# Kernel tuning notes

Hardware: AMD Instinct MI355X
Metric: run time of the kernel (lower is better)

## Reference

```python
import jax, jax.numpy as jnp
import numpy as np

R = 14        # num_relations
N = 100000    # num nodes
E = 1600000   # num edges
B = 8         # n_bases: num_blocks for layer 1, num_bases for layer 2
DIN, DH, DOUT = 64, 64, 64


def setup_inputs() -> dict:
    key = jax.random.key(0)
    ks = jax.random.split(key, 10)
    x = jax.random.normal(ks[0], (N, DIN), jnp.float32)
    edge_index = jax.random.randint(ks[1], (2, E), 0, N)
    edge_type = jax.random.randint(ks[2], (E,), 0, R)
    # Layer 1: block-diagonal decomposition weights (R, B, DIN/B, DH/B)
    w1 = jax.random.normal(ks[3], (R, B, DIN // B, DH // B), jnp.float32) * 0.1
    root1 = jax.random.normal(ks[4], (DIN, DH), jnp.float32) * 0.1
    bias1 = jnp.zeros((DH,), jnp.float32)
    # Layer 2: basis decomposition: W_r = sum_b comp2[r,b] * bases2[b]
    comp2 = jax.random.normal(ks[5], (R, B), jnp.float32) * 0.3
    bases2 = jax.random.normal(ks[6], (B, DH, DOUT), jnp.float32) * 0.1
    root2 = jax.random.normal(ks[7], (DH, DOUT), jnp.float32) * 0.1
    bias2 = jnp.zeros((DOUT,), jnp.float32)
    return {"x": x, "edge_index": edge_index, "edge_type": edge_type,
            "w1": w1, "root1": root1, "bias1": bias1,
            "comp2": comp2, "bases2": bases2, "root2": root2, "bias2": bias2}


def _rel_scatter_max(h_rel, src, dst, edge_type):
    """h_rel: (R, N, d) per-relation transformed node features.
    Per-relation scatter-max over destination nodes, then sum over relations
    (PyG RGCNConv with aggr='max': empty segments contribute 0)."""
    msgs = h_rel[edge_type, src]                  # (E, d) gather
    seg = edge_type * N + dst                     # combined (relation, dst) key
    agg = jax.ops.segment_max(msgs, seg, num_segments=R * N)  # (R*N, d), -inf where empty
    agg = jnp.where(jnp.isneginf(agg), 0.0, agg)
    return agg.reshape(R, N, -1).sum(axis=0)      # (N, d)


def reference(x, edge_index, edge_type, w1, root1, bias1, comp2, bases2, root2, bias2):
    src, dst = edge_index[0], edge_index[1]
    # ---- layer 1: block-diagonal RGCNConv, aggr='max' ----
    xb = x.reshape(N, B, DIN // B)
    h = jnp.einsum('nbi,rbio->rnbo', xb, w1).reshape(R, N, DH)
    out = _rel_scatter_max(h, src, dst, edge_type) + x @ root1 + bias1
    x1 = jax.nn.relu(out)  # dropout p=0.4 is identity in eval mode
    # ---- layer 2: basis-decomposed RGCNConv, aggr='max' ----
    W2 = jnp.einsum('rb,bio->rio', comp2, bases2)  # (R, DH, DOUT)
    h2 = jnp.einsum('ni,rio->rno', x1, W2)         # (R, N, DOUT)
    out2 = _rel_scatter_max(h2, src, dst, edge_type) + x1 @ root2 + bias2
    return out2
```

## Files before the change

kernel.cpp:

```cpp
#include <hip/hip_runtime.h>
#include <math.h>

#define RNUM 14
#define NNODE 100000
#define ENUM 1600000
#define NBKT 196
#define NFINE 8192
#define NBLK1 ((ENUM + 8191) / 8192)
#define NT16 (NNODE / 16)
#define NTB ((NT16 + 15) / 16)
#define FRAGREL (RNUM + 1)
#define FRAGTOT (2 * FRAGREL * 4096)

typedef __attribute__((ext_vector_type(8))) short bf16x8;
typedef __attribute__((ext_vector_type(4))) float f32x4;

__device__ inline unsigned short f2bf(float f) {
    unsigned u = __builtin_bit_cast(unsigned, f);
    u += 0x7FFF + ((u >> 16) & 1);
    return (unsigned short)(u >> 16);
}
__device__ inline float bf2f(unsigned short h) {
    unsigned u = ((unsigned)h) << 16;
    return __builtin_bit_cast(float, u);
}
__device__ inline int uload(const int* __restrict__ p) {
    return __builtin_amdgcn_readfirstlane(*p);
}

__global__ void __launch_bounds__(1024) bhist_k(const int* __restrict__ dst,
                                                int* __restrict__ bcnt) {
    __shared__ int c[256];
    int t = threadIdx.x;
    if (t < 256) c[t] = 0;
    __syncthreads();
    int e0 = blockIdx.x * 8192;
#pragma unroll
    for (int j = 0; j < 8; j++) {
        int e = e0 + j * 1024 + t;
        if (e < ENUM) atomicAdd(&c[dst[e] >> 9], 1);
    }
    __syncthreads();
    if (t < NBKT && c[t] > 0) atomicAdd(&bcnt[t], c[t]);
}

__global__ void bscan_k(const int* __restrict__ bcnt, int* __restrict__ bbase,
                        int* __restrict__ bcursor) {
    __shared__ int sh[256];
    int t = threadIdx.x;
    int v = (t < NBKT) ? bcnt[t] : 0;
    sh[t] = v;
    __syncthreads();
    for (int o = 1; o < 256; o <<= 1) {
        int u = (t >= o) ? sh[t - o] : 0;
        __syncthreads();
        sh[t] += u;
        __syncthreads();
    }
    int excl = sh[t] - v;
    if (t < NBKT) { bbase[t] = excl; bcursor[t] = excl; }
    if (t == NBKT - 1) bbase[NBKT] = sh[t];
}

__global__ void __launch_bounds__(1024) scatter1_k(const int* __restrict__ src,
        const int* __restrict__ dst, const int* __restrict__ et,
        int* __restrict__ bcursor, int2* __restrict__ pay) {
    __shared__ int cnt[256];
    __shared__ int rnk[256];
    __shared__ int base[256];
    int t = threadIdx.x;
    if (t < 256) { cnt[t] = 0; rnk[t] = 0; }
    __syncthreads();
    int e0 = blockIdx.x * 8192;
    int d[8], s[8], r[8];
#pragma unroll
    for (int j = 0; j < 8; j++) {
        int e = e0 + j * 1024 + t;
        if (e < ENUM) {
            d[j] = dst[e]; s[j] = src[e]; r[j] = et[e];
            atomicAdd(&cnt[d[j] >> 9], 1);
        } else d[j] = -1;
    }
    __syncthreads();
    if (t < NBKT && cnt[t] > 0) base[t] = atomicAdd(&bcursor[t], cnt[t]);
    __syncthreads();
#pragma unroll
    for (int j = 0; j < 8; j++) {
        if (d[j] < 0) continue;
        int b = d[j] >> 9;
        int rk = atomicAdd(&rnk[b], 1);
        int2 p; p.x = r[j] * NNODE + s[j]; p.y = (d[j] & 511) * 16 + r[j];
        pay[base[b] + rk] = p;
    }
}

__global__ void __launch_bounds__(1024) bsort_k(const int2* __restrict__ pay,
        const int* __restrict__ bbase, int* __restrict__ offs, int* __restrict__ ssrc) {
    __shared__ int cnt[NFINE];
    __shared__ int tsum[1024];
    int bkt = blockIdx.x, t = threadIdx.x;
    int e0 = bbase[bkt], e1 = bbase[bkt + 1];
#pragma unroll
    for (int i = t; i < NFINE; i += 1024) cnt[i] = 0;
    __syncthreads();
    for (int e = e0 + t; e < e1; e += 1024) atomicAdd(&cnt[pay[e].y], 1);
    __syncthreads();
    int loc[8], s = 0;
#pragma unroll
    for (int j = 0; j < 8; j++) { loc[j] = cnt[t * 8 + j]; s += loc[j]; }
    tsum[t] = s;
    __syncthreads();
    for (int o = 1; o < 1024; o <<= 1) {
        int u = (t >= o) ? tsum[t - o] : 0;
        __syncthreads();
        tsum[t] += u;
        __syncthreads();
    }
    int run = tsum[t] - s;
#pragma unroll
    for (int j = 0; j < 8; j++) {
        int idx = t * 8 + j;
        cnt[idx] = run;
        offs[bkt * NFINE + idx] = e0 + run;
        run += loc[j];
    }
    __syncthreads();
    for (int e = e0 + t; e < e1; e += 1024) {
        int2 p = pay[e];
        int rk = atomicAdd(&cnt[p.y], 1);
        ssrc[e0 + rk] = p.x;
    }
}

__global__ void prep_k(const float* __restrict__ w1, const float* __restrict__ comp2,
                       const float* __restrict__ bases2, const float* __restrict__ root1,
                       const float* __restrict__ root2, const float* __restrict__ x,
                       unsigned short* __restrict__ frag1, unsigned short* __restrict__ frag2,
                       unsigned short* __restrict__ xb) {
    int gid = blockIdx.x * 256 + threadIdx.x;
    if (gid < FRAGTOT) {
        int half = gid >= FRAGREL * 4096;
        int idx = gid - half * (FRAGREL * 4096);
        int j = idx & 7, lane = (idx >> 3) & 63, ot = (idx >> 9) & 3, kh = (idx >> 11) & 1, r = idx >> 12;
        int k = kh * 32 + (lane >> 4) * 8 + j;
        int c = ot * 16 + (lane & 15);
        float v;
        if (!half) {
            if (r < RNUM) {
                int bi = k >> 3, bo = c >> 3;
                v = 0.f;
                if (bi == bo) v = w1[((r * 8 + bi) * 8 + (k & 7)) * 8 + (c & 7)];
            } else v = root1[k * 64 + c];
            frag1[idx] = f2bf(v);
        } else {
            if (r < RNUM) {
                float s = 0.f;
#pragma unroll
                for (int b = 0; b < 8; b++) s += comp2[r * 8 + b] * bases2[(b * 64 + k) * 64 + c];
                v = s;
            } else v = root2[k * 64 + c];
            frag2[idx] = f2bf(v);
        }
    } else {
        int idx = gid - FRAGTOT;
        if (idx < NNODE * 64) xb[idx] = f2bf(x[idx]);
    }
}

__global__ void __launch_bounds__(256) gemm_k(const unsigned short* __restrict__ A,
                                              const unsigned short* __restrict__ F,
                                              const unsigned short* __restrict__ Froot,
                                              unsigned short* __restrict__ H,
                                              unsigned short* __restrict__ xrootb,
                                              int nrel) {
    int tb = blockIdx.x % NTB;
    int r  = blockIdx.x / NTB;
    bool isroot = (r == nrel);
    const unsigned short* Fr = isroot ? Froot : F + (size_t)r * 4096;
    int wave = threadIdx.x >> 6, lane = threadIdx.x & 63;
    bf16x8 wf[2][4];
#pragma unroll
    for (int kh = 0; kh < 2; kh++)
#pragma unroll
        for (int ot = 0; ot < 4; ot++)
            wf[kh][ot] = *(const bf16x8*)(Fr + ((kh * 4 + ot) * 64 + lane) * 8);
    int node16 = lane & 15;
    int kcol = (lane >> 4) * 8;
    int g = lane >> 4;
    unsigned short* Ybase = isroot ? xrootb : H + (size_t)r * NNODE * 64;
    for (int s = 0; s < 4; s++) {
        int nt = tb * 16 + wave * 4 + s;
        if (nt >= NT16) break;
        int nbase = nt * 16;
        const unsigned short* Arow = A + (size_t)(nbase + node16) * 64;
        bf16x8 b0 = *(const bf16x8*)(Arow + kcol);
        bf16x8 b1 = *(const bf16x8*)(Arow + 32 + kcol);
        f32x4 acc[4];
#pragma unroll
        for (int ot = 0; ot < 4; ot++) {
            acc[ot] = (f32x4){0.f, 0.f, 0.f, 0.f};
            acc[ot] = __builtin_amdgcn_mfma_f32_16x16x32_bf16(wf[0][ot], b0, acc[ot], 0, 0, 0);
            acc[ot] = __builtin_amdgcn_mfma_f32_16x16x32_bf16(wf[1][ot], b1, acc[ot], 0, 0, 0);
        }
        unsigned short* Yr = Ybase + (size_t)nbase * 64;
#pragma unroll
        for (int ot = 0; ot < 4; ot++) {
            unsigned p0 = (unsigned)f2bf(acc[ot][0]) | ((unsigned)f2bf(acc[ot][1]) << 16);
            unsigned p1 = (unsigned)f2bf(acc[ot][2]) | ((unsigned)f2bf(acc[ot][3]) << 16);
            uint2 pv; pv.x = p0; pv.y = p1;
            *(uint2*)(Yr + (size_t)node16 * 64 + ot * 16 + g * 4) = pv;
        }
    }
}

template <int RC>
__global__ void __launch_bounds__(256) agg_k(
    const unsigned short* __restrict__ H, const int* __restrict__ offs,
    const int* __restrict__ ssrc, const unsigned short* __restrict__ xrootb,
    const float* __restrict__ bias, float* __restrict__ aggbuf,
    unsigned short* __restrict__ x1b, float* __restrict__ outf,
    int r0, int r0N, int rcnt, int flags) {
    int wv = threadIdx.x >> 6, lane = threadIdx.x & 63;
    int d = __builtin_amdgcn_readfirstlane(blockIdx.x * 4 + wv);
    if (d >= NNODE) return;
    float msum = 0.f;

    if constexpr (RC > 0) {
        const int base = d * 16 + r0;
        int bnd[RC + 1];
#pragma unroll
        for (int j = 0; j <= RC; j++) bnd[j] = offs[base + j];
        int e0   = __builtin_amdgcn_readfirstlane(bnd[0]);
        int eend = __builtin_amdgcn_readfirstlane(bnd[RC]);
        float m = -INFINITY;
        for (int cb = e0; cb < eend; cb += 64) {
            int idx = cb + lane;
            int cidx = (idx < eend) ? idx : eend - 1;
            int sv = ssrc[cidx];
            unsigned long long mask = 0;
#pragma unroll
            for (int j = 1; j < RC; j++) {
                int kk_ = bnd[j] - cb;
                if (kk_ >= 0 && kk_ < 64 && bnd[j] > e0) mask |= 1ull << kk_;
            }
            int n = eend - cb; if (n > 64) n = 64;
            for (int k0 = 0; k0 < n; k0 += 32) {
                float h[32];
#pragma unroll
                for (int u = 0; u < 32; u++) {
                    int kk = k0 + u;
                    int kc = (kk < n) ? kk : n - 1;
                    int s = __builtin_amdgcn_readlane(sv, kc);
                    h[u] = bf2f(H[(size_t)(s - r0N) * 64 + lane]);
                }
#pragma unroll
                for (int u = 0; u < 32; u++) {
                    int kk = k0 + u;
                    if (kk >= n) break;
                    bool fl = (mask >> kk) & 1;
                    msum += fl ? m : 0.f;
                    m = fl ? h[u] : fmaxf(m, h[u]);
                }
            }
        }
        if (eend > e0) msum += m;
    } else {
        const int base = d * 16 + r0;
        for (int j = 0; j < rcnt; j++) {
            int e = uload(offs + base + j);
            int ee = uload(offs + base + j + 1);
            if (e >= ee) continue;
            float m = -INFINITY;
            for (; e < ee; e++) {
                int s = uload(ssrc + e);
                m = fmaxf(m, bf2f(H[(size_t)(s - r0N) * 64 + lane]));
            }
            msum += m;
        }
    }

    size_t o = (size_t)d * 64 + lane;
    if (!(flags & 1)) msum += aggbuf[o];
    if (!(flags & 2)) { aggbuf[o] = msum; return; }
    float v = msum + bf2f(xrootb[o]) + bias[lane];
    if (flags & 4) x1b[o] = f2bf(fmaxf(v, 0.f));
    else outf[o] = v;
}

extern "C" void kernel_launch(void* const* d_in, const int* in_sizes, int n_in,
                              void* d_out, int out_size, void* d_ws, size_t ws_size,
                              hipStream_t stream) {
    const float* x      = (const float*)d_in[0];
    const int*   ei     = (const int*)d_in[1];
    const int*   et     = (const int*)d_in[2];
    const float* w1     = (const float*)d_in[3];
    const float* root1  = (const float*)d_in[4];
    const float* bias1  = (const float*)d_in[5];
    const float* comp2  = (const float*)d_in[6];
    const float* bases2 = (const float*)d_in[7];
    const float* root2  = (const float*)d_in[8];
    const float* bias2  = (const float*)d_in[9];
    const int* srcv = ei;
    const int* dstv = ei + ENUM;
    float* out = (float*)d_out;

    char* w = (char*)d_ws;
    size_t off = 0;
    auto alloc = [&](size_t bytes) -> void* {
        void* p = w + off;
        off += (bytes + 255) & ~(size_t)255;
        return p;
    };
    int*   offs    = (int*)alloc(((size_t)NBKT * NFINE + 1) * sizeof(int));
    int*   bcnt    = (int*)alloc(256 * sizeof(int));
    int*   bbase   = (int*)alloc(257 * sizeof(int));
    int*   bcursor = (int*)alloc(256 * sizeof(int));
    int2*  pay     = (int2*)alloc((size_t)ENUM * sizeof(int2));
    int*   ssrc    = (int*)alloc((size_t)ENUM * sizeof(int));
    unsigned short* xb     = (unsigned short*)alloc((size_t)NNODE * 64 * 2);
    unsigned short* xrootb = (unsigned short*)alloc((size_t)NNODE * 64 * 2);
    unsigned short* frag1  = (unsigned short*)alloc((size_t)FRAGREL * 4096 * 2);
    unsigned short* frag2  = (unsigned short*)alloc((size_t)FRAGREL * 4096 * 2);
    size_t fixed = off;
    if (fixed > ws_size) return;
    size_t slab = ((size_t)NNODE * 64 * 2 + 255) & ~(size_t)255;
    size_t avail = ws_size - fixed;
    int r_per;
    float* aggbuf;
    unsigned short* H;
    if (avail >= (size_t)RNUM * slab) {
        r_per = RNUM;
        H = (unsigned short*)alloc((size_t)RNUM * slab);
        aggbuf = (float*)H;
    } else {
        aggbuf = (float*)alloc((size_t)NNODE * 64 * 4);
        if (off > ws_size) return;
        avail = ws_size - off;
        r_per = (int)(avail / slab);
        if (r_per < 1) return;
        if (r_per > RNUM) r_per = RNUM;
        H = (unsigned short*)alloc((size_t)r_per * slab);
    }

    hipMemsetAsync(bcnt, 0, 256 * sizeof(int), stream);

    bhist_k<<<NBLK1, 1024, 0, stream>>>(dstv, bcnt);
    bscan_k<<<1, 256, 0, stream>>>(bcnt, bbase, bcursor);
    scatter1_k<<<NBLK1, 1024, 0, stream>>>(srcv, dstv, et, bcursor, pay);
    bsort_k<<<NBKT, 1024, 0, stream>>>(pay, bbase, offs, ssrc);

    prep_k<<<(FRAGTOT + NNODE * 64 + 255) / 256, 256, 0, stream>>>(
        w1, comp2, bases2, root1, root2, x, frag1, frag2, xb);

    int nch = (RNUM + r_per - 1) / r_per;
    int aggGrid = NNODE / 4;

    for (int layer = 0; layer < 2; layer++) {
        const unsigned short* frag = layer ? frag2 : frag1;
        const unsigned short* rootf = (layer ? frag2 : frag1) + (size_t)RNUM * 4096;
        const float* bias = layer ? bias2 : bias1;
        for (int c = 0; c < nch; c++) {
            int r0 = c * r_per;
            int rcnt = (RNUM - r0 < r_per) ? (RNUM - r0) : r_per;
            int grid = (c == 0) ? (rcnt + 1) * NTB : rcnt * NTB;
            gemm_k<<<grid, 256, 0, stream>>>(xb, frag + (size_t)r0 * 4096, rootf,
                                             H, xrootb, rcnt);
            int flags = (c == 0 ? 1 : 0) | (c == nch - 1 ? 2 : 0) | (layer == 0 ? 4 : 0);
            if (rcnt == RNUM)
                agg_k<RNUM><<<aggGrid, 256, 0, stream>>>(H, offs, ssrc, xrootb, bias,
                                                         aggbuf, xb, out, r0, r0 * NNODE, rcnt, flags);
            else
                agg_k<0><<<aggGrid, 256, 0, stream>>>(H, offs, ssrc, xrootb, bias,
                                                      aggbuf, xb, out, r0, r0 * NNODE, rcnt, flags);
        }
    }
}
```

Baseline: 422.9 us.

## Use fixed per-bucket slots, LDS-staged gemm stores, nontemporal gathers, smaller unroll

```diff
diff --git a/kernel.cpp b/kernel.cpp
--- a/kernel.cpp
+++ b/kernel.cpp
@@ -6,6 +6,7 @@
 #define ENUM 1600000
 #define NBKT 196
 #define NFINE 8192
+#define SLOT 9216
 #define NBLK1 ((ENUM + 8191) / 8192)
 #define NT16 (NNODE / 16)
 #define NTB ((NT16 + 15) / 16)
@@ -28,43 +29,9 @@
     return __builtin_amdgcn_readfirstlane(*p);
 }
 
-__global__ void __launch_bounds__(1024) bhist_k(const int* __restrict__ dst,
-                                                int* __restrict__ bcnt) {
-    __shared__ int c[256];
-    int t = threadIdx.x;
-    if (t < 256) c[t] = 0;
-    __syncthreads();
-    int e0 = blockIdx.x * 8192;
-#pragma unroll
-    for (int j = 0; j < 8; j++) {
-        int e = e0 + j * 1024 + t;
-        if (e < ENUM) atomicAdd(&c[dst[e] >> 9], 1);
-    }
-    __syncthreads();
-    if (t < NBKT && c[t] > 0) atomicAdd(&bcnt[t], c[t]);
-}
-
-__global__ void bscan_k(const int* __restrict__ bcnt, int* __restrict__ bbase,
-                        int* __restrict__ bcursor) {
-    __shared__ int sh[256];
-    int t = threadIdx.x;
-    int v = (t < NBKT) ? bcnt[t] : 0;
-    sh[t] = v;
-    __syncthreads();
-    for (int o = 1; o < 256; o <<= 1) {
-        int u = (t >= o) ? sh[t - o] : 0;
-        __syncthreads();
-        sh[t] += u;
-        __syncthreads();
-    }
-    int excl = sh[t] - v;
-    if (t < NBKT) { bbase[t] = excl; bcursor[t] = excl; }
-    if (t == NBKT - 1) bbase[NBKT] = sh[t];
-}
-
 __global__ void __launch_bounds__(1024) scatter1_k(const int* __restrict__ src,
         const int* __restrict__ dst, const int* __restrict__ et,
-        int* __restrict__ bcursor, int2* __restrict__ pay) {
+        int* __restrict__ bcur, int2* __restrict__ pay) {
     __shared__ int cnt[256];
     __shared__ int rnk[256];
     __shared__ int base[256];
@@ -82,28 +49,31 @@
         } else d[j] = -1;
     }
     __syncthreads();
-    if (t < NBKT && cnt[t] > 0) base[t] = atomicAdd(&bcursor[t], cnt[t]);
+    if (t < NBKT && cnt[t] > 0) base[t] = atomicAdd(&bcur[t], cnt[t]);
     __syncthreads();
 #pragma unroll
     for (int j = 0; j < 8; j++) {
         if (d[j] < 0) continue;
         int b = d[j] >> 9;
         int rk = atomicAdd(&rnk[b], 1);
+        int pos = base[b] + rk;
+        if (pos >= SLOT) pos = SLOT - 1;
         int2 p; p.x = r[j] * NNODE + s[j]; p.y = (d[j] & 511) * 16 + r[j];
-        pay[base[b] + rk] = p;
+        pay[(size_t)b * SLOT + pos] = p;
     }
 }
 
 __global__ void __launch_bounds__(1024) bsort_k(const int2* __restrict__ pay,
-        const int* __restrict__ bbase, int* __restrict__ offs, int* __restrict__ ssrc) {
+        const int* __restrict__ bcur, int* __restrict__ offs, int* __restrict__ ssrc) {
     __shared__ int cnt[NFINE];
     __shared__ int tsum[1024];
     int bkt = blockIdx.x, t = threadIdx.x;
-    int e0 = bbase[bkt], e1 = bbase[bkt + 1];
+    int e0 = bkt * SLOT;
+    int ecnt = uload(bcur + bkt);
 #pragma unroll
     for (int i = t; i < NFINE; i += 1024) cnt[i] = 0;
     __syncthreads();
-    for (int e = e0 + t; e < e1; e += 1024) atomicAdd(&cnt[pay[e].y], 1);
+    for (int e = t; e < ecnt; e += 1024) atomicAdd(&cnt[pay[(size_t)e0 + e].y], 1);
     __syncthreads();
     int loc[8], s = 0;
 #pragma unroll
@@ -125,8 +95,8 @@
         run += loc[j];
     }
     __syncthreads();
-    for (int e = e0 + t; e < e1; e += 1024) {
-        int2 p = pay[e];
+    for (int e = t; e < ecnt; e += 1024) {
+        int2 p = pay[(size_t)e0 + e];
         int rk = atomicAdd(&cnt[p.y], 1);
         ssrc[e0 + rk] = p.x;
     }
@@ -167,12 +137,14 @@
     }
 }
 
+template <int TSTORE>
 __global__ void __launch_bounds__(256) gemm_k(const unsigned short* __restrict__ A,
                                               const unsigned short* __restrict__ F,
                                               const unsigned short* __restrict__ Froot,
                                               unsigned short* __restrict__ H,
                                               unsigned short* __restrict__ xrootb,
                                               int nrel) {
+    __shared__ unsigned short tl[4][16][72];
     int tb = blockIdx.x % NTB;
     int r  = blockIdx.x / NTB;
     bool isroot = (r == nrel);
@@ -203,17 +175,40 @@
             acc[ot] = __builtin_amdgcn_mfma_f32_16x16x32_bf16(wf[1][ot], b1, acc[ot], 0, 0, 0);
         }
         unsigned short* Yr = Ybase + (size_t)nbase * 64;
-#pragma unroll
-        for (int ot = 0; ot < 4; ot++) {
-            unsigned p0 = (unsigned)f2bf(acc[ot][0]) | ((unsigned)f2bf(acc[ot][1]) << 16);
-            unsigned p1 = (unsigned)f2bf(acc[ot][2]) | ((unsigned)f2bf(acc[ot][3]) << 16);
-            uint2 pv; pv.x = p0; pv.y = p1;
-            *(uint2*)(Yr + (size_t)node16 * 64 + ot * 16 + g * 4) = pv;
-        }
-    }
-}
-
-template <int RC>
+        if constexpr (TSTORE) {
+#pragma unroll
+            for (int ot = 0; ot < 4; ot++) {
+                uint2 pv;
+                pv.x = (unsigned)f2bf(acc[ot][0]) | ((unsigned)f2bf(acc[ot][1]) << 16);
+                pv.y = (unsigned)f2bf(acc[ot][2]) | ((unsigned)f2bf(acc[ot][3]) << 16);
+                *(uint2*)&tl[wave][node16][ot * 16 + g * 4] = pv;
+            }
+#pragma unroll
+            for (int q = 0; q < 2; q++) {
+                int nd = q * 8 + (lane >> 3);
+                int ch = (lane & 7) * 8;
+                uint4 v = *(uint4*)&tl[wave][nd][ch];
+                *(uint4*)(Yr + (size_t)nd * 64 + ch) = v;
+            }
+        } else {
+#pragma unroll
+            for (int ot = 0; ot < 4; ot++) {
+                uint2 pv;
+                pv.x = (unsigned)f2bf(acc[ot][0]) | ((unsigned)f2bf(acc[ot][1]) << 16);
+                pv.y = (unsigned)f2bf(acc[ot][2]) | ((unsigned)f2bf(acc[ot][3]) << 16);
+                *(uint2*)(Yr + (size_t)node16 * 64 + ot * 16 + g * 4) = pv;
+            }
+        }
+    }
+}
+
+template <bool NT>
+__device__ inline float hload(const unsigned short* __restrict__ p) {
+    unsigned short v = NT ? __builtin_nontemporal_load(p) : *p;
+    return bf2f(v);
+}
+
+template <int RC, bool NT>
 __global__ void __launch_bounds__(256) agg_k(
     const unsigned short* __restrict__ H, const int* __restrict__ offs,
     const int* __restrict__ ssrc, const unsigned short* __restrict__ xrootb,
@@ -244,17 +239,17 @@
                 if (kk_ >= 0 && kk_ < 64 && bnd[j] > e0) mask |= 1ull << kk_;
             }
             int n = eend - cb; if (n > 64) n = 64;
-            for (int k0 = 0; k0 < n; k0 += 32) {
-                float h[32];
-#pragma unroll
-                for (int u = 0; u < 32; u++) {
+            for (int k0 = 0; k0 < n; k0 += 16) {
+                float h[16];
+#pragma unroll
+                for (int u = 0; u < 16; u++) {
                     int kk = k0 + u;
                     int kc = (kk < n) ? kk : n - 1;
                     int s = __builtin_amdgcn_readlane(sv, kc);
-                    h[u] = bf2f(H[(size_t)(s - r0N) * 64 + lane]);
+                    h[u] = hload<NT>(H + (size_t)(s - r0N) * 64 + lane);
                 }
 #pragma unroll
-                for (int u = 0; u < 32; u++) {
+                for (int u = 0; u < 16; u++) {
                     int kk = k0 + u;
                     if (kk >= n) break;
                     bool fl = (mask >> kk) & 1;
@@ -311,12 +306,10 @@
         off += (bytes + 255) & ~(size_t)255;
         return p;
     };
-    int*   offs    = (int*)alloc(((size_t)NBKT * NFINE + 1) * sizeof(int));
-    int*   bcnt    = (int*)alloc(256 * sizeof(int));
-    int*   bbase   = (int*)alloc(257 * sizeof(int));
-    int*   bcursor = (int*)alloc(256 * sizeof(int));
-    int2*  pay     = (int2*)alloc((size_t)ENUM * sizeof(int2));
-    int*   ssrc    = (int*)alloc((size_t)ENUM * sizeof(int));
+    int*   offs = (int*)alloc(((size_t)NBKT * NFINE + 1) * sizeof(int));
+    int*   bcur = (int*)alloc(256 * sizeof(int));
+    int2*  pay  = (int2*)alloc((size_t)NBKT * SLOT * sizeof(int2));
+    int*   ssrc = (int*)alloc((size_t)NBKT * SLOT * sizeof(int));
     unsigned short* xb     = (unsigned short*)alloc((size_t)NNODE * 64 * 2);
     unsigned short* xrootb = (unsigned short*)alloc((size_t)NNODE * 64 * 2);
     unsigned short* frag1  = (unsigned short*)alloc((size_t)FRAGREL * 4096 * 2);
@@ -342,12 +335,10 @@
         H = (unsigned short*)alloc((size_t)r_per * slab);
     }
 
-    hipMemsetAsync(bcnt, 0, 256 * sizeof(int), stream);
-
-    bhist_k<<<NBLK1, 1024, 0, stream>>>(dstv, bcnt);
-    bscan_k<<<1, 256, 0, stream>>>(bcnt, bbase, bcursor);
-    scatter1_k<<<NBLK1, 1024, 0, stream>>>(srcv, dstv, et, bcursor, pay);
-    bsort_k<<<NBKT, 1024, 0, stream>>>(pay, bbase, offs, ssrc);
+    hipMemsetAsync(bcur, 0, 256 * sizeof(int), stream);
+
+    scatter1_k<<<NBLK1, 1024, 0, stream>>>(srcv, dstv, et, bcur, pay);
+    bsort_k<<<NBKT, 1024, 0, stream>>>(pay, bcur, offs, ssrc);
 
     prep_k<<<(FRAGTOT + NNODE * 64 + 255) / 256, 256, 0, stream>>>(
         w1, comp2, bases2, root1, root2, x, frag1, frag2, xb);
@@ -363,15 +354,24 @@
             int r0 = c * r_per;
             int rcnt = (RNUM - r0 < r_per) ? (RNUM - r0) : r_per;
             int grid = (c == 0) ? (rcnt + 1) * NTB : rcnt * NTB;
-            gemm_k<<<grid, 256, 0, stream>>>(xb, frag + (size_t)r0 * 4096, rootf,
-                                             H, xrootb, rcnt);
+            if (layer == 0)
+                gemm_k<1><<<grid, 256, 0, stream>>>(xb, frag + (size_t)r0 * 4096, rootf,
+                                                    H, xrootb, rcnt);
+            else
+                gemm_k<0><<<grid, 256, 0, stream>>>(xb, frag + (size_t)r0 * 4096, rootf,
+                                                    H, xrootb, rcnt);
             int flags = (c == 0 ? 1 : 0) | (c == nch - 1 ? 2 : 0) | (layer == 0 ? 4 : 0);
-            if (rcnt == RNUM)
-                agg_k<RNUM><<<aggGrid, 256, 0, stream>>>(H, offs, ssrc, xrootb, bias,
-                                                         aggbuf, xb, out, r0, r0 * NNODE, rcnt, flags);
-            else
-                agg_k<0><<<aggGrid, 256, 0, stream>>>(H, offs, ssrc, xrootb, bias,
-                                                      aggbuf, xb, out, r0, r0 * NNODE, rcnt, flags);
-        }
-    }
-}
+            if (rcnt == RNUM) {
+                if (layer == 0)
+                    agg_k<RNUM, true><<<aggGrid, 256, 0, stream>>>(H, offs, ssrc, xrootb, bias,
+                                                                   aggbuf, xb, out, r0, r0 * NNODE, rcnt, flags);
+                else
+                    agg_k<RNUM, false><<<aggGrid, 256, 0, stream>>>(H, offs, ssrc, xrootb, bias,
+                                                                    aggbuf, xb, out, r0, r0 * NNODE, rcnt, flags);
+            } else {
+                agg_k<0, false><<<aggGrid, 256, 0, stream>>>(H, offs, ssrc, xrootb, bias,
+                                                             aggbuf, xb, out, r0, r0 * NNODE, rcnt, flags);
+            }
+        }
+    }
+}
```

Measured after the change: 388.0 us. 8.2% less time.
